# Kernel tuning notes

Measured on AMD Instinct MI355X. Metric: run time of the kernel, lower is better.

## Reference

```python
import jax, jax.numpy as jnp
import numpy as np
from jax import lax

B, T_ENC, IN, H, V, EMB = 128, 512, 2, 256, 29, 8


def _gru_cell(x_t, h, Wih, Whh, bih, bhh):
    # PyTorch GRU cell, gate order (r, z, n)
    gi = x_t @ Wih.T + bih            # [B, 3H]
    gh = h @ Whh.T + bhh              # [B, 3H]
    ir, iz, inn = jnp.split(gi, 3, axis=-1)
    hr, hz, hn = jnp.split(gh, 3, axis=-1)
    r = jax.nn.sigmoid(ir + hr)
    z = jax.nn.sigmoid(iz + hz)
    n = jnp.tanh(inn + r * hn)
    return (1.0 - z) * n + z * h


def _gru_scan(xs, Wih, Whh, bih, bhh, reverse):
    # xs: [B, T, D] -> outputs [B, T, H], final hidden [B, H]
    h0 = jnp.zeros((xs.shape[0], Whh.shape[-1]), xs.dtype)
    def step(h, x_t):
        h = _gru_cell(x_t, h, Wih, Whh, bih, bhh)
        return h, h
    hT, ys = lax.scan(step, h0, jnp.swapaxes(xs, 0, 1), reverse=reverse)
    return jnp.swapaxes(ys, 0, 1), hT


def _forward(x, target_seq, eWih0, eWhh0, ebih0, ebhh0, eWih1, eWhh1, ebih1, ebhh1,
             e2d_W, e2d_b, dWih0, dWih1, dWhh, dbih, dbhh, q_W, q_b, out_W, out_b, emb):
    # ---- bidirectional 2-layer GRU encoder ----
    yf0, hf0 = _gru_scan(x, eWih0[0], eWhh0[0], ebih0[0], ebhh0[0], False)
    yb0, hb0 = _gru_scan(x, eWih0[1], eWhh0[1], ebih0[1], ebhh0[1], True)
    y0 = jnp.concatenate([yf0, yb0], axis=-1)          # [B, T, 2H]
    yf1, hf1 = _gru_scan(y0, eWih1[0], eWhh1[0], ebih1[0], ebhh1[0], False)
    yb1, hb1 = _gru_scan(y0, eWih1[1], eWhh1[1], ebih1[1], ebhh1[1], True)
    y1 = jnp.concatenate([yf1, yb1], axis=-1)          # [B, T, 2H]
    enc_out = y1 @ e2d_W.T + e2d_b                     # [B, T, H]
    # hidden.reshape(L, 2, B, H).sum(dim=1): fwd + bwd per layer
    h0c = hf0 + hb0
    h1c = hf1 + hb1

    max_steps = target_seq.shape[1] - 1
    init_tok = target_seq[:, 0]

    def dec_step(carry, _):
        h0, h1, tok = carry
        e = emb[tok]                                   # [B, EMB]
        h0 = _gru_cell(e, h0, dWih0, dWhh[0], dbih[0], dbhh[0])
        h1 = _gru_cell(h0, h1, dWih1, dWhh[1], dbih[1], dbhh[1])
        q = h1 @ q_W.T + q_b                           # [B, H]
        scores = jnp.einsum('bte,be->bt', enc_out, q)  # [B, T]
        w = jax.nn.softmax(scores, axis=1)
        ctx = jnp.einsum('bt,bte->be', w, enc_out)     # [B, H]
        logits = (h1 + ctx) @ out_W.T + out_b          # [B, V] (dropout is identity in eval)
        tok = jnp.argmax(logits, axis=-1)
        return (h0, h1, tok), logits

    (h0c, h1c, _), logits = lax.scan(dec_step, (h0c, h1c, init_tok), None, length=max_steps)
    logits = jnp.swapaxes(logits, 0, 1)                # [B, max_steps, V]
    hidden = jnp.stack([h0c, h1c], axis=0)             # [L, B, H]
    return logits, hidden


def setup_inputs() -> dict:
    key = jax.random.key(0)
    ks = jax.random.split(key, 24)
    def p(k, *shape):
        return jax.random.normal(k, shape, jnp.float32) * 0.05
    return {
        'x': jax.random.normal(ks[0], (B, T_ENC, IN), jnp.float32),
        'target_seq': jax.random.randint(ks[1], (B, 64), 0, V),
        'eWih0': p(ks[2], 2, 3 * H, IN),
        'eWhh0': p(ks[3], 2, 3 * H, H),
        'ebih0': p(ks[4], 2, 3 * H),
        'ebhh0': p(ks[5], 2, 3 * H),
        'eWih1': p(ks[6], 2, 3 * H, 2 * H),
        'eWhh1': p(ks[7], 2, 3 * H, H),
        'ebih1': p(ks[8], 2, 3 * H),
        'ebhh1': p(ks[9], 2, 3 * H),
        'e2d_W': p(ks[10], H, 2 * H),
        'e2d_b': p(ks[11], H),
        'dWih0': p(ks[12], 3 * H, EMB),
        'dWih1': p(ks[13], 3 * H, H),
        'dWhh': p(ks[14], 2, 3 * H, H),
        'dbih': p(ks[15], 2, 3 * H),
        'dbhh': p(ks[16], 2, 3 * H),
        'q_W': p(ks[17], H, H),
        'q_b': p(ks[18], H),
        'out_W': p(ks[19], V, H),
        'out_b': p(ks[20], V),
        'emb': p(ks[21], V, EMB),
    }


def reference(x, target_seq, eWih0, eWhh0, ebih0, ebhh0, eWih1, eWhh1, ebih1, ebhh1,
              e2d_W, e2d_b, dWih0, dWih1, dWhh, dbih, dbhh, q_W, q_b, out_W, out_b, emb):
    return _forward(x, target_seq, eWih0, eWhh0, ebih0, ebhh0, eWih1, eWhh1, ebih1, ebhh1,
                    e2d_W, e2d_b, dWih0, dWih1, dWhh, dbih, dbhh, q_W, q_b, out_W, out_b, emb)
```

## Files before the change

kernel.cpp:

```cpp
#include <hip/hip_runtime.h>
#include <hip/hip_bf16.h>
#include <hip/hip_fp16.h>
#include <stdint.h>

#define BB 128
#define TT 512
#define HH 256
#define VV 29
#define NSTEP 63
#define BT (BB*TT)
#define CHUNK 64

typedef _Float16 f16;
typedef _Float16 f16x2 __attribute__((ext_vector_type(2)));
typedef _Float16 f16x8 __attribute__((ext_vector_type(8)));
typedef float f32x4 __attribute__((ext_vector_type(4)));

static __device__ __forceinline__ float fdot2u(uint32_t a, uint32_t b, float c) {
  return __builtin_amdgcn_fdot2(__builtin_bit_cast(f16x2, a),
                                __builtin_bit_cast(f16x2, b), c, false);
}
static __device__ __forceinline__ float sigm_(float x) {
  return 1.0f / (1.0f + __expf(-x));
}

__global__ void k_cvt(const float* __restrict__ s, f16* __restrict__ d, int n) {
  int i = blockIdx.x * 256 + threadIdx.x;
  if (i < n) d[i] = (f16)s[i];
}

template<int LAYER>
__global__ __launch_bounds__(512, 2)
void k_scan(const float* __restrict__ x,
            const f16* __restrict__ gi,
            const uint32_t* __restrict__ whh,
            const float* __restrict__ wih0,
            const float* __restrict__ bih,
            const float* __restrict__ bhh,
            f16* __restrict__ y,
            float* __restrict__ hstate,
            int t0, int nsteps)
{
  const int wg = blockIdx.x, b = wg >> 1, dir = wg & 1;
  const int tid = threadIdx.x, pair = tid >> 1, half = tid & 1;
  __shared__ __align__(16) uint4 hv4[32];

  uint4 w0[16], w1[16], w2[16];
  {
    const uint32_t* wp = whh + (size_t)dir * 768 * 128;
    const uint4* r0 = (const uint4*)(wp + (size_t)pair * 128 + half * 64);
    const uint4* r1 = (const uint4*)(wp + (size_t)(pair + 256) * 128 + half * 64);
    const uint4* r2 = (const uint4*)(wp + (size_t)(pair + 512) * 128 + half * 64);
#pragma unroll
    for (int i = 0; i < 16; i++) { w0[i] = r0[i]; w1[i] = r1[i]; w2[i] = r2[i]; }
  }
  const float bh0 = bhh[dir * 768 + pair];
  const float bh1 = bhh[dir * 768 + pair + 256];
  const float bh2 = bhh[dir * 768 + pair + 512];
  float bi0 = 0, bi1 = 0, bi2 = 0;
  float wi00 = 0, wi01 = 0, wi10 = 0, wi11 = 0, wi20 = 0, wi21 = 0;
  if (LAYER == 0) {
    bi0 = bih[dir * 768 + pair];
    bi1 = bih[dir * 768 + pair + 256];
    bi2 = bih[dir * 768 + pair + 512];
    wi00 = wih0[(dir * 768 + pair) * 2 + 0];
    wi01 = wih0[(dir * 768 + pair) * 2 + 1];
    wi10 = wih0[(dir * 768 + pair + 256) * 2 + 0];
    wi11 = wih0[(dir * 768 + pair + 256) * 2 + 1];
    wi20 = wih0[(dir * 768 + pair + 512) * 2 + 0];
    wi21 = wih0[(dir * 768 + pair + 512) * 2 + 1];
  }
  float* hs = hstate + ((size_t)dir * BB + b) * 256;
  float hreg = hs[pair];
  if (tid < 128) {
    f16x2 p2; p2[0] = (f16)hs[2 * tid]; p2[1] = (f16)hs[2 * tid + 1];
    ((uint32_t*)hv4)[tid] = __builtin_bit_cast(uint32_t, p2);
  }
  __syncthreads();

  const uint4* hw = hv4 + half * 16;
  for (int s = 0; s < nsteps; ++s) {
    const int t = dir ? (TT - 1 - t0 - s) : (t0 + s);
    float gr, gz, gn;
    if (LAYER == 0) {
      float x0 = x[((size_t)b * TT + t) * 2 + 0];
      float x1 = x[((size_t)b * TT + t) * 2 + 1];
      gr = wi00 * x0 + wi01 * x1 + bi0;
      gz = wi10 * x0 + wi11 * x1 + bi1;
      gn = wi20 * x0 + wi21 * x1 + bi2;
    } else {
      const f16* g = gi + ((size_t)b * nsteps + s) * 1536 + dir * 768 + pair;
      gr = (float)g[0]; gz = (float)g[256]; gn = (float)g[512];
    }
    float a0 = 0.f, a1 = 0.f, a2 = 0.f;
#pragma unroll
    for (int j = 0; j < 16; ++j) {
      uint4 hh = hw[j];
      a0 = fdot2u(w0[j].x, hh.x, a0); a0 = fdot2u(w0[j].y, hh.y, a0);
      a0 = fdot2u(w0[j].z, hh.z, a0); a0 = fdot2u(w0[j].w, hh.w, a0);
      a1 = fdot2u(w1[j].x, hh.x, a1); a1 = fdot2u(w1[j].y, hh.y, a1);
      a1 = fdot2u(w1[j].z, hh.z, a1); a1 = fdot2u(w1[j].w, hh.w, a1);
      a2 = fdot2u(w2[j].x, hh.x, a2); a2 = fdot2u(w2[j].y, hh.y, a2);
      a2 = fdot2u(w2[j].z, hh.z, a2); a2 = fdot2u(w2[j].w, hh.w, a2);
    }
    a0 += __shfl_xor(a0, 1);
    a1 += __shfl_xor(a1, 1);
    a2 += __shfl_xor(a2, 1);

    float r = sigm_(gr + a0 + bh0);
    float z = sigm_(gz + a1 + bh1);
    float n = tanhf(gn + r * (a2 + bh2));
    float hn = (1.0f - z) * n + z * hreg;
    hreg = hn;
    if (half == 0) y[((size_t)b * TT + t) * 512 + dir * 256 + pair] = (f16)hn;
    __syncthreads();
    if (half == 0) ((f16*)hv4)[pair] = (f16)hn;
    __syncthreads();
  }
  if (half == 0) hs[pair] = hreg;
}

__global__ __launch_bounds__(256)
void k_gemm(const f16* __restrict__ A, const f16* __restrict__ Bt,
            f16* __restrict__ C, const float* __restrict__ bias,
            int K, int shift, long bstride, int inner, int ldc, int coloff)
{
  const int m0 = blockIdx.x * 64, n0 = blockIdx.y * 64;
  const int tid = threadIdx.x, lane = tid & 63, wv = tid >> 6;
  __shared__ __align__(16) f16 As[64 * 40];
  __shared__ __align__(16) f16 Bs[64 * 40];
  f32x4 acc[4] = {{0,0,0,0},{0,0,0,0},{0,0,0,0},{0,0,0,0}};
  const int lrow = tid >> 2, lseg = tid & 3;
  const int ml = lane & 15, quad = lane >> 4;
  const int r = m0 + lrow;
  const f16* arow = A + (long)(r >> shift) * bstride
                      + (long)(r & ((1 << shift) - 1)) * inner;
  const f16* brow = Bt + (size_t)(n0 + lrow) * K;
  for (int k0 = 0; k0 < K; k0 += 32) {
    uint4 av = *(const uint4*)(arow + k0 + lseg * 8);
    uint4 bv = *(const uint4*)(brow + k0 + lseg * 8);
    __syncthreads();
    *(uint4*)(As + lrow * 40 + lseg * 8) = av;
    *(uint4*)(Bs + lrow * 40 + lseg * 8) = bv;
    __syncthreads();
    f16x8 af = *(const f16x8*)(As + (wv * 16 + ml) * 40 + quad * 8);
#pragma unroll
    for (int ns = 0; ns < 4; ++ns) {
      f16x8 bf = *(const f16x8*)(Bs + (ns * 16 + ml) * 40 + quad * 8);
      acc[ns] = __builtin_amdgcn_mfma_f32_16x16x32_f16(af, bf, acc[ns], 0, 0, 0);
    }
  }
#pragma unroll
  for (int ns = 0; ns < 4; ++ns) {
#pragma unroll
    for (int rr = 0; rr < 4; ++rr) {
      int row = m0 + wv * 16 + quad * 4 + rr;
      int col = n0 + ns * 16 + ml;
      float v = acc[ns][rr];
      if (bias) v += bias[col];
      C[(size_t)row * ldc + coloff + col] = (f16)v;
    }
  }
}

static __device__ __forceinline__ void mv3(const f16* __restrict__ W, int row0,
                                           const uint4* __restrict__ hsh,
                                           float& g0, float& g1, float& g2) {
  const uint4* w0 = (const uint4*)(W + (size_t)row0 * 256);
  const uint4* w1 = (const uint4*)(W + (size_t)(row0 + 256) * 256);
  const uint4* w2 = (const uint4*)(W + (size_t)(row0 + 512) * 256);
#pragma unroll 2
  for (int kc = 0; kc < 8; ++kc) {
    uint4 hq[4], aq[4], bq[4], cq[4];
#pragma unroll
    for (int j = 0; j < 4; ++j) {
      aq[j] = w0[4 * kc + j]; bq[j] = w1[4 * kc + j]; cq[j] = w2[4 * kc + j];
      hq[j] = hsh[4 * kc + j];
    }
#pragma unroll
    for (int j = 0; j < 4; ++j) {
      g0 = fdot2u(aq[j].x, hq[j].x, g0); g0 = fdot2u(aq[j].y, hq[j].y, g0);
      g0 = fdot2u(aq[j].z, hq[j].z, g0); g0 = fdot2u(aq[j].w, hq[j].w, g0);
      g1 = fdot2u(bq[j].x, hq[j].x, g1); g1 = fdot2u(bq[j].y, hq[j].y, g1);
      g1 = fdot2u(bq[j].z, hq[j].z, g1); g1 = fdot2u(bq[j].w, hq[j].w, g1);
      g2 = fdot2u(cq[j].x, hq[j].x, g2); g2 = fdot2u(cq[j].y, hq[j].y, g2);
      g2 = fdot2u(cq[j].z, hq[j].z, g2); g2 = fdot2u(cq[j].w, hq[j].w, g2);
    }
  }
}
static __device__ __forceinline__ float mv1(const f16* __restrict__ W, long row,
                                            const uint4* __restrict__ hsh, float g) {
  const uint4* w = (const uint4*)(W + (size_t)row * 256);
#pragma unroll 2
  for (int kc = 0; kc < 8; ++kc) {
    uint4 aq[4], hq[4];
#pragma unroll
    for (int j = 0; j < 4; ++j) { aq[j] = w[4 * kc + j]; hq[j] = hsh[4 * kc + j]; }
#pragma unroll
    for (int j = 0; j < 4; ++j) {
      g = fdot2u(aq[j].x, hq[j].x, g); g = fdot2u(aq[j].y, hq[j].y, g);
      g = fdot2u(aq[j].z, hq[j].z, g); g = fdot2u(aq[j].w, hq[j].w, g);
    }
  }
  return g;
}
static __device__ __forceinline__ float edot(uint4 w, const float* e) {
  f16x2 a = __builtin_bit_cast(f16x2, w.x);
  f16x2 b = __builtin_bit_cast(f16x2, w.y);
  f16x2 c = __builtin_bit_cast(f16x2, w.z);
  f16x2 d = __builtin_bit_cast(f16x2, w.w);
  return (float)a[0]*e[0] + (float)a[1]*e[1] + (float)b[0]*e[2] + (float)b[1]*e[3]
       + (float)c[0]*e[4] + (float)c[1]*e[5] + (float)d[0]*e[6] + (float)d[1]*e[7];
}

__global__ __launch_bounds__(256)
void k_decoder(const f16* __restrict__ dwhh,
               const f16* __restrict__ dwih1,
               const f16* __restrict__ dwih0,
               const f16* __restrict__ qw,
               const f16* __restrict__ outw,
               const f16* __restrict__ enc,
               const float* __restrict__ dbih,
               const float* __restrict__ dbhh,
               const float* __restrict__ qb, const float* __restrict__ outb,
               const float* __restrict__ emb,
               const float* __restrict__ hs0, const float* __restrict__ hs1,
               const int* __restrict__ tseq,
               float* __restrict__ out)
{
  const int b = blockIdx.x, tid = threadIdx.x;
  __shared__ __align__(16) f16 h0sh[256], h1sh[256], qsh[256];
  __shared__ float sc[512];
  __shared__ float red[4];
  __shared__ __align__(16) float hc[256];
  __shared__ __align__(16) float cpart[2][256];
  __shared__ float lg[32];
  __shared__ float e8[8];
  __shared__ int toksh;

  h0sh[tid] = (f16)(hs0[b * 256 + tid] + hs0[32768 + b * 256 + tid]);
  h1sh[tid] = (f16)(hs1[b * 256 + tid] + hs1[32768 + b * 256 + tid]);
  if (tid == 0) toksh = tseq[b * 64];
  __syncthreads();

  for (int s = 0; s < NSTEP; ++s) {
    if (tid < 8) e8[tid] = emb[toksh * 8 + tid];
    uint4 wq0 = *(const uint4*)(dwih0 + (size_t)tid * 8);
    uint4 wq1 = *(const uint4*)(dwih0 + (size_t)(tid + 256) * 8);
    uint4 wq2 = *(const uint4*)(dwih0 + (size_t)(tid + 512) * 8);
    float g0 = dbhh[tid], g1 = dbhh[tid + 256], g2 = dbhh[tid + 512];
    mv3(dwhh, tid, (const uint4*)h0sh, g0, g1, g2);
    __syncthreads();
    {
      float i0 = dbih[tid]       + edot(wq0, e8);
      float i1 = dbih[tid + 256] + edot(wq1, e8);
      float i2 = dbih[tid + 512] + edot(wq2, e8);
      float r = sigm_(i0 + g0);
      float z = sigm_(i1 + g1);
      float n = tanhf(i2 + r * g2);
      float hp = (float)h0sh[tid];
      h0sh[tid] = (f16)((1.f - z) * n + z * hp);
    }
    __syncthreads();

    float a0 = dbih[768 + tid], a1 = dbih[768 + tid + 256], a2 = dbih[768 + tid + 512];
    mv3(dwih1, tid, (const uint4*)h0sh, a0, a1, a2);
    float b0 = dbhh[768 + tid], b1 = dbhh[768 + tid + 256], b2 = dbhh[768 + tid + 512];
    mv3(dwhh + (size_t)768 * 256, tid, (const uint4*)h1sh, b0, b1, b2);
    float h1new;
    {
      float r = sigm_(a0 + b0);
      float z = sigm_(a1 + b1);
      float n = tanhf(a2 + r * b2);
      float hp = (float)h1sh[tid];
      h1new = (1.f - z) * n + z * hp;
    }
    __syncthreads();
    h1sh[tid] = (f16)h1new;
    __syncthreads();

    qsh[tid] = (f16)mv1(qw, tid, (const uint4*)h1sh, qb[tid]);
    __syncthreads();

#pragma unroll
    for (int pass = 0; pass < 2; ++pass) {
      int t = tid + pass * 256;
      sc[t] = mv1(enc, (size_t)b * 512 + t, (const uint4*)qsh, 0.f);
    }
    __syncthreads();

    float mloc = fmaxf(sc[tid], sc[tid + 256]);
#pragma unroll
    for (int off = 32; off; off >>= 1) mloc = fmaxf(mloc, __shfl_xor(mloc, off));
    if ((tid & 63) == 0) red[tid >> 6] = mloc;
    __syncthreads();
    float m = fmaxf(fmaxf(red[0], red[1]), fmaxf(red[2], red[3]));
    float ex0 = __expf(sc[tid] - m), ex1 = __expf(sc[tid + 256] - m);
    __syncthreads();
    sc[tid] = ex0; sc[tid + 256] = ex1;
    float lloc = ex0 + ex1;
#pragma unroll
    for (int off = 32; off; off >>= 1) lloc += __shfl_xor(lloc, off);
    if ((tid & 63) == 0) red[tid >> 6] = lloc;
    __syncthreads();
    float l = red[0] + red[1] + red[2] + red[3];

    {
      const int c2 = tid & 127, th = tid >> 7;
      const uint32_t* eb = (const uint32_t*)enc + (((size_t)b * 512 + th * 256) * 128) + c2;
      const float* wsc = sc + th * 256;
      float c0 = 0.f, c1 = 0.f;
#pragma unroll 8
      for (int i = 0; i < 256; ++i) {
        uint32_t v = eb[(size_t)i * 128];
        float wgt = wsc[i];
        f16x2 h2 = __builtin_bit_cast(f16x2, v);
        c0 += wgt * (float)h2[0];
        c1 += wgt * (float)h2[1];
      }
      ((float2*)cpart[th])[c2] = float2{c0, c1};
    }
    __syncthreads();
    hc[tid] = (cpart[0][tid] + cpart[1][tid]) / l + (float)h1sh[tid];
    __syncthreads();

    if (tid < VV * 8) {
      const int v = tid >> 3, kseg = tid & 7;
      float acc = 0.f;
      const uint4* ow = (const uint4*)(outw + (size_t)v * 256 + kseg * 32);
      const float4* hv = (const float4*)(hc + kseg * 32);
#pragma unroll
      for (int j = 0; j < 4; ++j) {
        uint4 wq = ow[j];
        float4 ha = hv[2 * j], hb = hv[2 * j + 1];
        f16x2 p0 = __builtin_bit_cast(f16x2, wq.x);
        f16x2 p1 = __builtin_bit_cast(f16x2, wq.y);
        f16x2 p2 = __builtin_bit_cast(f16x2, wq.z);
        f16x2 p3 = __builtin_bit_cast(f16x2, wq.w);
        acc += (float)p0[0]*ha.x + (float)p0[1]*ha.y + (float)p1[0]*ha.z + (float)p1[1]*ha.w;
        acc += (float)p2[0]*hb.x + (float)p2[1]*hb.y + (float)p3[0]*hb.z + (float)p3[1]*hb.w;
      }
      acc += __shfl_xor(acc, 1);
      acc += __shfl_xor(acc, 2);
      acc += __shfl_xor(acc, 4);
      if (kseg == 0) {
        float lv = acc + outb[v];
        lg[v] = lv;
        out[((size_t)b * NSTEP + s) * VV + v] = lv;
      }
    }
    __syncthreads();
    if (tid == 0) {
      int best = 0; float bv = lg[0];
      for (int v = 1; v < VV; ++v) if (lg[v] > bv) { bv = lg[v]; best = v; }
      toksh = best;
    }
    __syncthreads();
  }

  out[233856 + b * 256 + tid] = (float)h0sh[tid];
  out[233856 + 32768 + b * 256 + tid] = (float)h1sh[tid];
}

extern "C" void kernel_launch(void* const* d_in, const int* in_sizes, int n_in,
                              void* d_out, int out_size, void* d_ws, size_t ws_size,
                              hipStream_t stream) {
  (void)in_sizes; (void)n_in; (void)out_size; (void)ws_size;
  const float* x     = (const float*)d_in[0];
  const int*   tseq  = (const int*)d_in[1];
  const float* eWih0 = (const float*)d_in[2];
  const float* eWhh0 = (const float*)d_in[3];
  const float* ebih0 = (const float*)d_in[4];
  const float* ebhh0 = (const float*)d_in[5];
  const float* eWih1 = (const float*)d_in[6];
  const float* eWhh1 = (const float*)d_in[7];
  const float* ebih1 = (const float*)d_in[8];
  const float* ebhh1 = (const float*)d_in[9];
  const float* e2dW  = (const float*)d_in[10];
  const float* e2db  = (const float*)d_in[11];
  const float* dWih0 = (const float*)d_in[12];
  const float* dWih1 = (const float*)d_in[13];
  const float* dWhh  = (const float*)d_in[14];
  const float* dbih  = (const float*)d_in[15];
  const float* dbhh  = (const float*)d_in[16];
  const float* qW    = (const float*)d_in[17];
  const float* qb    = (const float*)d_in[18];
  const float* outW  = (const float*)d_in[19];
  const float* outb  = (const float*)d_in[20];
  const float* emb   = (const float*)d_in[21];

  uint8_t* ws = (uint8_t*)d_ws;
  size_t o = 0;
  auto take = [&](size_t bytes) -> void* {
    void* p = ws + o;
    o += (bytes + 255) & ~(size_t)255;
    return p;
  };
  f16* whh0_16  = (f16*)take((size_t)2 * 768 * 256 * 2);
  f16* whh1_16  = (f16*)take((size_t)2 * 768 * 256 * 2);
  f16* wih1_16  = (f16*)take((size_t)2 * 768 * 512 * 2);
  f16* e2d_16   = (f16*)take((size_t)256 * 512 * 2);
  f16* qw_16    = (f16*)take((size_t)256 * 256 * 2);
  f16* outw_16  = (f16*)take((size_t)29 * 256 * 2);
  f16* dwih0_16 = (f16*)take((size_t)768 * 8 * 2);
  f16* dwih1_16 = (f16*)take((size_t)768 * 256 * 2);
  f16* dwhh_16  = (f16*)take((size_t)2 * 768 * 256 * 2);
  f16* y0   = (f16*)take((size_t)BT * 512 * 2);
  f16* y1   = (f16*)take((size_t)BT * 512 * 2);
  f16* gi   = (f16*)take((size_t)BB * CHUNK * 1536 * 2);
  float* hs0 = (float*)take((size_t)2 * BB * 256 * 4);
  float* hs1 = (float*)take((size_t)2 * BB * 256 * 4);
  f16* enc = y0;

  hipMemsetAsync(hs0, 0, (size_t)2 * BB * 256 * 4, stream);
  hipMemsetAsync(hs1, 0, (size_t)2 * BB * 256 * 4, stream);

  auto cvt = [&](const float* s, f16* d, int n) {
    k_cvt<<<(n + 255) / 256, 256, 0, stream>>>(s, d, n);
  };
  cvt(eWhh0, whh0_16, 2 * 768 * 256);
  cvt(eWhh1, whh1_16, 2 * 768 * 256);
  cvt(eWih1, wih1_16, 2 * 768 * 512);
  cvt(e2dW,  e2d_16,  256 * 512);
  cvt(qW,    qw_16,   256 * 256);
  cvt(outW,  outw_16, 29 * 256);
  cvt(dWih0, dwih0_16, 768 * 8);
  cvt(dWih1, dwih1_16, 768 * 256);
  cvt(dWhh,  dwhh_16, 2 * 768 * 256);

  k_scan<0><<<256, 512, 0, stream>>>(x, nullptr, (const uint32_t*)whh0_16,
                                     eWih0, ebih0, ebhh0, y0, hs0, 0, TT);

  const long BSTR = (long)TT * 512;
  for (int c = 0; c < TT / CHUNK; ++c) {
    const int t0 = c * CHUNK;
    k_gemm<<<dim3(BB * CHUNK / 64, 12), 256, 0, stream>>>(
        y0 + (size_t)t0 * 512, wih1_16, gi, ebih1,
        512, 6, BSTR, 512, 1536, 0);
    k_gemm<<<dim3(BB * CHUNK / 64, 12), 256, 0, stream>>>(
        y0 + (size_t)(TT - 1 - t0) * 512, wih1_16 + (size_t)768 * 512, gi, ebih1 + 768,
        512, 6, BSTR, -512, 1536, 768);
    k_scan<1><<<256, 512, 0, stream>>>(nullptr, gi, (const uint32_t*)whh1_16,
                                       nullptr, nullptr, ebhh1, y1, hs1, t0, CHUNK);
  }

  k_gemm<<<dim3(BT / 64, 4), 256, 0, stream>>>(y1, e2d_16, enc, e2db,
                                               512, 30, 0, 512, 256, 0);

  k_decoder<<<128, 256, 0, stream>>>(dwhh_16, dwih1_16, dwih0_16, qw_16, outw_16,
                                     enc, dbih, dbhh, qb, outb, emb,
                                     hs0, hs1, tseq, (float*)d_out);
}
```

Baseline: 5.571 ms.

## Widen decoder blocks to 768 threads, one gate row per thread

The decoder kernel now launches 768 threads per batch block instead of 256, so each thread computes one gate row rather than three. The two hidden-to-hidden matvecs for both layers are issued together, since layer 1's recurrent term does not depend on the new h0. The q projection is split into K-halves, and attention scores and context are spread over 512 threads. The embedding fetch moves into the argmax thread. This aims to cut the serial per-step latency of the 63-step decoder loop, which runs on only 128 blocks, at the cost of extra shared-memory staging and synchronisation.

New measurement: 5.640 ms. No clear change (+1.2%).

```diff
diff --git a/kernel.cpp b/kernel.cpp
--- a/kernel.cpp
+++ b/kernel.cpp
@@ -163,44 +163,25 @@
   }
 }
 
-static __device__ __forceinline__ void mv3(const f16* __restrict__ W, int row0,
-                                           const uint4* __restrict__ hsh,
-                                           float& g0, float& g1, float& g2) {
-  const uint4* w0 = (const uint4*)(W + (size_t)row0 * 256);
-  const uint4* w1 = (const uint4*)(W + (size_t)(row0 + 256) * 256);
-  const uint4* w2 = (const uint4*)(W + (size_t)(row0 + 512) * 256);
-#pragma unroll 2
-  for (int kc = 0; kc < 8; ++kc) {
-    uint4 hq[4], aq[4], bq[4], cq[4];
-#pragma unroll
-    for (int j = 0; j < 4; ++j) {
-      aq[j] = w0[4 * kc + j]; bq[j] = w1[4 * kc + j]; cq[j] = w2[4 * kc + j];
-      hq[j] = hsh[4 * kc + j];
-    }
-#pragma unroll
-    for (int j = 0; j < 4; ++j) {
-      g0 = fdot2u(aq[j].x, hq[j].x, g0); g0 = fdot2u(aq[j].y, hq[j].y, g0);
-      g0 = fdot2u(aq[j].z, hq[j].z, g0); g0 = fdot2u(aq[j].w, hq[j].w, g0);
-      g1 = fdot2u(bq[j].x, hq[j].x, g1); g1 = fdot2u(bq[j].y, hq[j].y, g1);
-      g1 = fdot2u(bq[j].z, hq[j].z, g1); g1 = fdot2u(bq[j].w, hq[j].w, g1);
-      g2 = fdot2u(cq[j].x, hq[j].x, g2); g2 = fdot2u(cq[j].y, hq[j].y, g2);
-      g2 = fdot2u(cq[j].z, hq[j].z, g2); g2 = fdot2u(cq[j].w, hq[j].w, g2);
-    }
-  }
-}
-static __device__ __forceinline__ float mv1(const f16* __restrict__ W, long row,
-                                            const uint4* __restrict__ hsh, float g) {
-  const uint4* w = (const uint4*)(W + (size_t)row * 256);
-#pragma unroll 2
-  for (int kc = 0; kc < 8; ++kc) {
-    uint4 aq[4], hq[4];
-#pragma unroll
-    for (int j = 0; j < 4; ++j) { aq[j] = w[4 * kc + j]; hq[j] = hsh[4 * kc + j]; }
-#pragma unroll
-    for (int j = 0; j < 4; ++j) {
-      g = fdot2u(aq[j].x, hq[j].x, g); g = fdot2u(aq[j].y, hq[j].y, g);
-      g = fdot2u(aq[j].z, hq[j].z, g); g = fdot2u(aq[j].w, hq[j].w, g);
-    }
+static __device__ __forceinline__ float dot256(const uint4* __restrict__ w,
+                                               const uint4* __restrict__ h) {
+  float g = 0.f;
+#pragma unroll 8
+  for (int j = 0; j < 32; ++j) {
+    uint4 a = w[j], b = h[j];
+    g = fdot2u(a.x, b.x, g); g = fdot2u(a.y, b.y, g);
+    g = fdot2u(a.z, b.z, g); g = fdot2u(a.w, b.w, g);
+  }
+  return g;
+}
+static __device__ __forceinline__ float dot128(const uint4* __restrict__ w,
+                                               const uint4* __restrict__ h) {
+  float g = 0.f;
+#pragma unroll 8
+  for (int j = 0; j < 16; ++j) {
+    uint4 a = w[j], b = h[j];
+    g = fdot2u(a.x, b.x, g); g = fdot2u(a.y, b.y, g);
+    g = fdot2u(a.z, b.z, g); g = fdot2u(a.w, b.w, g);
   }
   return g;
 }
@@ -213,7 +194,7 @@
        + (float)c[0]*e[4] + (float)c[1]*e[5] + (float)d[0]*e[6] + (float)d[1]*e[7];
 }
 
-__global__ __launch_bounds__(256)
+__global__ __launch_bounds__(768, 3)
 void k_decoder(const f16* __restrict__ dwhh,
                const f16* __restrict__ dwih1,
                const f16* __restrict__ dwih0,
@@ -230,104 +211,136 @@
 {
   const int b = blockIdx.x, tid = threadIdx.x;
   __shared__ __align__(16) f16 h0sh[256], h1sh[256], qsh[256];
+  __shared__ float h1f[256];
+  __shared__ float g0sh[768], g1sh[768], gi0n[256], gi1sh[768];
+  __shared__ float qpart[2][256];
   __shared__ float sc[512];
-  __shared__ float red[4];
+  __shared__ float redm[12], redl[12];
+  __shared__ __align__(16) float cpart[4][256];
   __shared__ __align__(16) float hc[256];
-  __shared__ __align__(16) float cpart[2][256];
   __shared__ float lg[32];
   __shared__ float e8[8];
   __shared__ int toksh;
 
-  h0sh[tid] = (f16)(hs0[b * 256 + tid] + hs0[32768 + b * 256 + tid]);
-  h1sh[tid] = (f16)(hs1[b * 256 + tid] + hs1[32768 + b * 256 + tid]);
-  if (tid == 0) toksh = tseq[b * 64];
+  if (tid < 256) {
+    h0sh[tid] = (f16)(hs0[b * 256 + tid] + hs0[32768 + b * 256 + tid]);
+    h1sh[tid] = (f16)(hs1[b * 256 + tid] + hs1[32768 + b * 256 + tid]);
+  }
+  if (tid == 0) {
+    int tk = tseq[b * 64]; toksh = tk;
+    for (int k = 0; k < 8; ++k) e8[k] = emb[tk * 8 + k];
+  }
   __syncthreads();
 
+  const int wvi = tid >> 6;
+
   for (int s = 0; s < NSTEP; ++s) {
-    if (tid < 8) e8[tid] = emb[toksh * 8 + tid];
-    uint4 wq0 = *(const uint4*)(dwih0 + (size_t)tid * 8);
-    uint4 wq1 = *(const uint4*)(dwih0 + (size_t)(tid + 256) * 8);
-    uint4 wq2 = *(const uint4*)(dwih0 + (size_t)(tid + 512) * 8);
-    float g0 = dbhh[tid], g1 = dbhh[tid + 256], g2 = dbhh[tid + 512];
-    mv3(dwhh, tid, (const uint4*)h0sh, g0, g1, g2);
-    __syncthreads();
     {
-      float i0 = dbih[tid]       + edot(wq0, e8);
-      float i1 = dbih[tid + 256] + edot(wq1, e8);
-      float i2 = dbih[tid + 512] + edot(wq2, e8);
-      float r = sigm_(i0 + g0);
-      float z = sigm_(i1 + g1);
-      float n = tanhf(i2 + r * g2);
+      const uint4* wA = (const uint4*)(dwhh + (size_t)tid * 256);
+      const uint4* wB = (const uint4*)(dwhh + (size_t)(768 + tid) * 256);
+      const uint4* h0q = (const uint4*)h0sh;
+      const uint4* h1q = (const uint4*)h1sh;
+      float gA = dbhh[tid], gB = dbhh[768 + tid];
+#pragma unroll 8
+      for (int j = 0; j < 32; ++j) {
+        uint4 a = wA[j], ha = h0q[j];
+        uint4 c = wB[j], hb = h1q[j];
+        gA = fdot2u(a.x, ha.x, gA); gA = fdot2u(a.y, ha.y, gA);
+        gA = fdot2u(a.z, ha.z, gA); gA = fdot2u(a.w, ha.w, gA);
+        gB = fdot2u(c.x, hb.x, gB); gB = fdot2u(c.y, hb.y, gB);
+        gB = fdot2u(c.z, hb.z, gB); gB = fdot2u(c.w, hb.w, gB);
+      }
+      uint4 wi = *(const uint4*)(dwih0 + (size_t)tid * 8);
+      float gi = dbih[tid] + edot(wi, e8);
+      if (tid < 512) g0sh[tid] = gA + gi;
+      else { g0sh[tid] = gA; gi0n[tid - 512] = gi; }
+      g1sh[tid] = gB;
+    }
+    __syncthreads();
+
+    if (tid < 256) {
+      float r = sigm_(g0sh[tid]);
+      float z = sigm_(g0sh[tid + 256]);
+      float n = tanhf(gi0n[tid] + r * g0sh[tid + 512]);
       float hp = (float)h0sh[tid];
       h0sh[tid] = (f16)((1.f - z) * n + z * hp);
     }
     __syncthreads();
 
-    float a0 = dbih[768 + tid], a1 = dbih[768 + tid + 256], a2 = dbih[768 + tid + 512];
-    mv3(dwih1, tid, (const uint4*)h0sh, a0, a1, a2);
-    float b0 = dbhh[768 + tid], b1 = dbhh[768 + tid + 256], b2 = dbhh[768 + tid + 512];
-    mv3(dwhh + (size_t)768 * 256, tid, (const uint4*)h1sh, b0, b1, b2);
-    float h1new;
-    {
-      float r = sigm_(a0 + b0);
-      float z = sigm_(a1 + b1);
-      float n = tanhf(a2 + r * b2);
+    gi1sh[tid] = dbih[768 + tid] +
+                 dot256((const uint4*)(dwih1 + (size_t)tid * 256), (const uint4*)h0sh);
+    __syncthreads();
+
+    if (tid < 256) {
+      float r = sigm_(gi1sh[tid] + g1sh[tid]);
+      float z = sigm_(gi1sh[tid + 256] + g1sh[tid + 256]);
+      float n = tanhf(gi1sh[tid + 512] + r * g1sh[tid + 512]);
       float hp = (float)h1sh[tid];
-      h1new = (1.f - z) * n + z * hp;
-    }
-    __syncthreads();
-    h1sh[tid] = (f16)h1new;
-    __syncthreads();
-
-    qsh[tid] = (f16)mv1(qw, tid, (const uint4*)h1sh, qb[tid]);
-    __syncthreads();
-
-#pragma unroll
-    for (int pass = 0; pass < 2; ++pass) {
-      int t = tid + pass * 256;
-      sc[t] = mv1(enc, (size_t)b * 512 + t, (const uint4*)qsh, 0.f);
-    }
-    __syncthreads();
-
-    float mloc = fmaxf(sc[tid], sc[tid + 256]);
+      float hn = (1.f - z) * n + z * hp;
+      h1f[tid] = hn;
+      h1sh[tid] = (f16)hn;
+    }
+    __syncthreads();
+
+    if (tid < 512) {
+      int row = tid & 255, kh = tid >> 8;
+      qpart[kh][row] = dot128((const uint4*)(qw + (size_t)row * 256 + kh * 128),
+                              (const uint4*)h1sh + kh * 16);
+    }
+    __syncthreads();
+    if (tid < 256) qsh[tid] = (f16)(qpart[0][tid] + qpart[1][tid] + qb[tid]);
+    __syncthreads();
+
+    if (tid < 512)
+      sc[tid] = dot256((const uint4*)(enc + ((size_t)b * 512 + tid) * 256),
+                       (const uint4*)qsh);
+    __syncthreads();
+
+    float v = (tid < 512) ? sc[tid] : -1e30f;
+    float mloc = v;
 #pragma unroll
     for (int off = 32; off; off >>= 1) mloc = fmaxf(mloc, __shfl_xor(mloc, off));
-    if ((tid & 63) == 0) red[tid >> 6] = mloc;
-    __syncthreads();
-    float m = fmaxf(fmaxf(red[0], red[1]), fmaxf(red[2], red[3]));
-    float ex0 = __expf(sc[tid] - m), ex1 = __expf(sc[tid + 256] - m);
-    __syncthreads();
-    sc[tid] = ex0; sc[tid + 256] = ex1;
-    float lloc = ex0 + ex1;
+    if ((tid & 63) == 0) redm[wvi] = mloc;
+    __syncthreads();
+    float m = redm[0];
+#pragma unroll
+    for (int i = 1; i < 12; ++i) m = fmaxf(m, redm[i]);
+    float e = 0.f;
+    if (tid < 512) { e = __expf(v - m); sc[tid] = e; }
+    float lloc = e;
 #pragma unroll
     for (int off = 32; off; off >>= 1) lloc += __shfl_xor(lloc, off);
-    if ((tid & 63) == 0) red[tid >> 6] = lloc;
-    __syncthreads();
-    float l = red[0] + red[1] + red[2] + red[3];
-
-    {
-      const int c2 = tid & 127, th = tid >> 7;
-      const uint32_t* eb = (const uint32_t*)enc + (((size_t)b * 512 + th * 256) * 128) + c2;
-      const float* wsc = sc + th * 256;
+    if ((tid & 63) == 0) redl[wvi] = lloc;
+    __syncthreads();
+    float l = redl[0];
+#pragma unroll
+    for (int i = 1; i < 12; ++i) l += redl[i];
+
+    if (tid < 512) {
+      const int c2 = tid & 127, seg = tid >> 7;
+      const uint32_t* eb = (const uint32_t*)enc + (((size_t)b * 512 + seg * 128) * 128) + c2;
+      const float* wsc = sc + seg * 128;
       float c0 = 0.f, c1 = 0.f;
 #pragma unroll 8
-      for (int i = 0; i < 256; ++i) {
-        uint32_t v = eb[(size_t)i * 128];
+      for (int i = 0; i < 128; ++i) {
+        uint32_t vv = eb[(size_t)i * 128];
         float wgt = wsc[i];
-        f16x2 h2 = __builtin_bit_cast(f16x2, v);
+        f16x2 h2 = __builtin_bit_cast(f16x2, vv);
         c0 += wgt * (float)h2[0];
         c1 += wgt * (float)h2[1];
       }
-      ((float2*)cpart[th])[c2] = float2{c0, c1};
-    }
-    __syncthreads();
-    hc[tid] = (cpart[0][tid] + cpart[1][tid]) / l + (float)h1sh[tid];
+      ((float2*)cpart[seg])[c2] = float2{c0, c1};
+    }
+    __syncthreads();
+    if (tid < 256)
+      hc[tid] = (cpart[0][tid] + cpart[1][tid] + cpart[2][tid] + cpart[3][tid]) / l
+                + h1f[tid];
     __syncthreads();
 
     if (tid < VV * 8) {
-      const int v = tid >> 3, kseg = tid & 7;
+      const int vv = tid >> 3, kseg = tid & 7;
       float acc = 0.f;
-      const uint4* ow = (const uint4*)(outw + (size_t)v * 256 + kseg * 32);
+      const uint4* ow = (const uint4*)(outw + (size_t)vv * 256 + kseg * 32);
       const float4* hv = (const float4*)(hc + kseg * 32);
 #pragma unroll
       for (int j = 0; j < 4; ++j) {
@@ -344,22 +357,25 @@
       acc += __shfl_xor(acc, 2);
       acc += __shfl_xor(acc, 4);
       if (kseg == 0) {
-        float lv = acc + outb[v];
-        lg[v] = lv;
-        out[((size_t)b * NSTEP + s) * VV + v] = lv;
+        float lv = acc + outb[vv];
+        lg[vv] = lv;
+        out[((size_t)b * NSTEP + s) * VV + vv] = lv;
       }
     }
     __syncthreads();
     if (tid == 0) {
       int best = 0; float bv = lg[0];
-      for (int v = 1; v < VV; ++v) if (lg[v] > bv) { bv = lg[v]; best = v; }
+      for (int v2 = 1; v2 < VV; ++v2) if (lg[v2] > bv) { bv = lg[v2]; best = v2; }
       toksh = best;
-    }
-    __syncthreads();
-  }
-
-  out[233856 + b * 256 + tid] = (float)h0sh[tid];
-  out[233856 + 32768 + b * 256 + tid] = (float)h1sh[tid];
+      for (int k = 0; k < 8; ++k) e8[k] = emb[best * 8 + k];
+    }
+    __syncthreads();
+  }
+
+  if (tid < 256) {
+    out[233856 + b * 256 + tid] = (float)h0sh[tid];
+    out[233856 + 32768 + b * 256 + tid] = (float)h1sh[tid];
+  }
 }
 
 extern "C" void kernel_launch(void* const* d_in, const int* in_sizes, int n_in,
@@ -447,7 +463,7 @@
   k_gemm<<<dim3(BT / 64, 4), 256, 0, stream>>>(y1, e2d_16, enc, e2db,
                                                512, 30, 0, 512, 256, 0);
 
-  k_decoder<<<128, 256, 0, stream>>>(dwhh_16, dwih1_16, dwih0_16, qw_16, outw_16,
+  k_decoder<<<128, 768, 0, stream>>>(dwhh_16, dwih1_16, dwih0_16, qw_16, outw_16,
                                      enc, dbih, dbhh, qb, outb, emb,
                                      hs0, hs1, tseq, (float*)d_out);
 }
```
